# Performance work log

Measured on AMD Instinct MI355X. Metric: run time of the kernel, lower is better.

Reference implementation:

```python
import jax, jax.numpy as jnp
import numpy as np

N, D, H, F = 50000, 128, 8, 512
HD = D // H
EPS_BN = 1e-5


def _batchnorm(x, gamma, beta):
    # BatchNorm1d in training mode: per-feature batch stats over node dim
    m = x.mean(axis=0)
    v = x.var(axis=0)
    return (x - m) * jax.lax.rsqrt(v + EPS_BN) * gamma + beta


def setup_inputs() -> dict:
    key = jax.random.key(0)
    ks = jax.random.split(key, 12)
    s = 0.05
    return {
        "src": jax.random.normal(ks[0], (N, D), jnp.float32),
        "edge_index": jax.random.randint(ks[1], (2, 800000), 0, N, jnp.int64),
        "q_w": jax.random.normal(ks[2], (D, D), jnp.float32) * s,
        "q_b": jnp.zeros((D,), jnp.float32),
        "k_w": jax.random.normal(ks[3], (D, D), jnp.float32) * s,
        "v_w": jax.random.normal(ks[4], (D, D), jnp.float32) * s,
        "out_w": jax.random.normal(ks[5], (D, D), jnp.float32) * s,
        "out_b": jnp.zeros((D,), jnp.float32),
        "g1": jnp.ones((D,), jnp.float32),
        "b1": jnp.zeros((D,), jnp.float32),
        "lin1_w": jax.random.normal(ks[6], (F, D), jnp.float32) * s,
        "lin1_b": jnp.zeros((F,), jnp.float32),
        "lin2_w": jax.random.normal(ks[7], (D, F), jnp.float32) * s,
        "lin2_b": jnp.zeros((D,), jnp.float32),
        "g2": jnp.ones((D,), jnp.float32),
        "b2": jnp.zeros((D,), jnp.float32),
    }


def reference(src, edge_index, q_w, q_b, k_w, v_w, out_w, out_b,
              g1, b1, lin1_w, lin1_b, lin2_w, lin2_b, g2, b2):
    n = src.shape[0]
    # add self loops, then attention edge index is (dst=edge[1], src=edge[0])
    loops = jnp.arange(n, dtype=edge_index.dtype)
    ei = jnp.concatenate([edge_index, jnp.stack([loops, loops])], axis=1)
    e_src, e_dst = ei[0], ei[1]  # message flows e_src -> e_dst; query index = e_dst

    scaling = float(HD) ** (-0.5)
    q = ((src @ q_w.T + q_b) * scaling).reshape(n, H, HD)
    k = (src @ k_w.T).reshape(n, H, HD)
    v = (src @ v_w.T).reshape(n, H, HD)

    # per-edge scores [E, H]
    w = jnp.einsum("ehd,ehd->eh", q[e_dst], k[e_src])
    # deterministic segment softmax over edges grouped by destination node
    mx = jax.ops.segment_max(w, e_dst, num_segments=n)
    ex = jnp.exp(w - mx[e_dst])
    den = jax.ops.segment_sum(ex, e_dst, num_segments=n)
    attn_w = ex / (den[e_dst] + 1e-16)  # [E, H]

    # weighted scatter-add aggregation -> [n, H, HD]
    msgs = attn_w[:, :, None] * v[e_src]
    agg = jax.ops.segment_sum(msgs, e_dst, num_segments=n)

    attn_out = agg.reshape(n, D) @ out_w.T + out_b
    x = _batchnorm(src + attn_out, g1, b1)

    ff = jax.nn.leaky_relu(x @ lin1_w.T + lin1_b, negative_slope=0.01)
    ff = ff @ lin2_w.T + lin2_b
    x = _batchnorm(x + ff, g2, b2)
    return x
```

## Files before the change

kernel.cpp:

```cpp
#include <hip/hip_runtime.h>
#include <math.h>

#define D 128
#define H 8
#define HD 16

typedef __attribute__((ext_vector_type(8))) short bf16x8;
typedef __attribute__((ext_vector_type(4))) float f32x4;

__device__ __forceinline__ ushort f2bf(float x) {
    union { float f; unsigned u; } v; v.f = x;
    unsigned r = v.u + 0x7fffu + ((v.u >> 16) & 1u);
    return (ushort)(r >> 16);
}
__device__ __forceinline__ float bflo(unsigned u) {
    union { unsigned u; float f; } x; x.u = u << 16; return x.f;
}
__device__ __forceinline__ float bfhi(unsigned u) {
    union { unsigned u; float f; } x; x.u = u & 0xffff0000u; return x.f;
}
__device__ __forceinline__ float bf2f(short s) {
    union { unsigned u; float f; } x; x.u = ((unsigned)(ushort)s) << 16; return x.f;
}

__device__ __forceinline__ float dot16(const float* qf, uint4 a, uint4 b) {
    float w;
    w  = qf[0]  * bflo(a.x) + qf[1]  * bfhi(a.x);
    w += qf[2]  * bflo(a.y) + qf[3]  * bfhi(a.y);
    w += qf[4]  * bflo(a.z) + qf[5]  * bfhi(a.z);
    w += qf[6]  * bflo(a.w) + qf[7]  * bfhi(a.w);
    w += qf[8]  * bflo(b.x) + qf[9]  * bfhi(b.x);
    w += qf[10] * bflo(b.y) + qf[11] * bfhi(b.y);
    w += qf[12] * bflo(b.z) + qf[13] * bfhi(b.z);
    w += qf[14] * bflo(b.w) + qf[15] * bfhi(b.w);
    return w;
}
__device__ __forceinline__ void acc16(float* num, float e, uint4 a, uint4 b) {
    num[0]  = fmaf(e, bflo(a.x), num[0]);  num[1]  = fmaf(e, bfhi(a.x), num[1]);
    num[2]  = fmaf(e, bflo(a.y), num[2]);  num[3]  = fmaf(e, bfhi(a.y), num[3]);
    num[4]  = fmaf(e, bflo(a.z), num[4]);  num[5]  = fmaf(e, bfhi(a.z), num[5]);
    num[6]  = fmaf(e, bflo(a.w), num[6]);  num[7]  = fmaf(e, bfhi(a.w), num[7]);
    num[8]  = fmaf(e, bflo(b.x), num[8]);  num[9]  = fmaf(e, bfhi(b.x), num[9]);
    num[10] = fmaf(e, bflo(b.y), num[10]); num[11] = fmaf(e, bfhi(b.y), num[11]);
    num[12] = fmaf(e, bflo(b.z), num[12]); num[13] = fmaf(e, bfhi(b.z), num[13]);
    num[14] = fmaf(e, bflo(b.w), num[14]); num[15] = fmaf(e, bfhi(b.w), num[15]);
}

template<int AMODE, int EPI, int K, int MW>
__global__ __launch_bounds__(256)
void gemm_v2_kernel(const void* __restrict__ Ap,
                    const ushort* __restrict__ W,
                    const float* __restrict__ bias,
                    const void* __restrict__ extra,
                    const float* __restrict__ stats,
                    ushort* __restrict__ outb,
                    int N)
{
    constexpr int M   = MW * 4;
    constexpr int KC  = (K < 128) ? K : 128;
    constexpr int KT  = KC / 32;
    constexpr int NKC = K / KC;

    const int lane = threadIdx.x & 63, wave = threadIdx.x >> 6;
    const int lr = lane & 15, lq = lane >> 4;
    const int row0 = blockIdx.x * 32;
    const int c0w  = wave * MW;

    int ar0 = row0 + lr;      if (ar0 > N - 1) ar0 = N - 1;
    int ar1 = row0 + 16 + lr; if (ar1 > N - 1) ar1 = N - 1;

    bf16x8 afr[2][KT];

    auto loadA = [&](int kc) {
        #pragma unroll
        for (int s = 0; s < 2; ++s) {
            int ar = s ? ar1 : ar0;
            if (AMODE == 0 || AMODE == 2) {
                const ushort* ap = (const ushort*)Ap + (size_t)ar * K + kc * KC + lq * 8;
                #pragma unroll
                for (int t = 0; t < KT; ++t) {
                    bf16x8 raw = *(const bf16x8*)(ap + t * 32);
                    if (AMODE == 0) {
                        afr[s][t] = raw;
                    } else {
                        int kb = kc * KC + t * 32 + lq * 8;
                        const float4* scp = (const float4*)(stats + 256 + kb);
                        const float4* shp = (const float4*)(stats + 384 + kb);
                        float4 sA = scp[0], sB = scp[1], hA = shp[0], hB = shp[1];
                        bf16x8 o;
                        o[0] = (short)f2bf(fmaf(bf2f(raw[0]), sA.x, hA.x));
                        o[1] = (short)f2bf(fmaf(bf2f(raw[1]), sA.y, hA.y));
                        o[2] = (short)f2bf(fmaf(bf2f(raw[2]), sA.z, hA.z));
                        o[3] = (short)f2bf(fmaf(bf2f(raw[3]), sA.w, hA.w));
                        o[4] = (short)f2bf(fmaf(bf2f(raw[4]), sB.x, hB.x));
                        o[5] = (short)f2bf(fmaf(bf2f(raw[5]), sB.y, hB.y));
                        o[6] = (short)f2bf(fmaf(bf2f(raw[6]), sB.z, hB.z));
                        o[7] = (short)f2bf(fmaf(bf2f(raw[7]), sB.w, hB.w));
                        afr[s][t] = o;
                    }
                }
            } else {
                const float* ap = (const float*)Ap + (size_t)ar * K + kc * KC + lq * 8;
                #pragma unroll
                for (int t = 0; t < KT; ++t) {
                    float4 f0 = *(const float4*)(ap + t * 32);
                    float4 f1 = *(const float4*)(ap + t * 32 + 4);
                    bf16x8 o;
                    o[0] = (short)f2bf(f0.x); o[1] = (short)f2bf(f0.y);
                    o[2] = (short)f2bf(f0.z); o[3] = (short)f2bf(f0.w);
                    o[4] = (short)f2bf(f1.x); o[5] = (short)f2bf(f1.y);
                    o[6] = (short)f2bf(f1.z); o[7] = (short)f2bf(f1.w);
                    afr[s][t] = o;
                }
            }
        }
    };

    if (NKC == 1) loadA(0);

    const float*  extf = (const float*)extra;
    const ushort* extb = (const ushort*)extra;

    #pragma unroll 1
    for (int cp = 0; cp < MW / 32; ++cp) {
        const int cbase = c0w + cp * 32;
        f32x4 acc[2][2] = {};

        #pragma unroll 1
        for (int kc = 0; kc < NKC; ++kc) {
            if (NKC > 1) loadA(kc);
            const ushort* wp0 = W + (size_t)(cbase + lr) * K + kc * KC + lq * 8;
            const ushort* wp1 = wp0 + (size_t)16 * K;
            #pragma unroll
            for (int t = 0; t < KT; ++t) {
                bf16x8 b0 = *(const bf16x8*)(wp0 + t * 32);
                bf16x8 b1 = *(const bf16x8*)(wp1 + t * 32);
                acc[0][0] = __builtin_amdgcn_mfma_f32_16x16x32_bf16(afr[0][t], b0, acc[0][0], 0, 0, 0);
                acc[1][0] = __builtin_amdgcn_mfma_f32_16x16x32_bf16(afr[1][t], b0, acc[1][0], 0, 0, 0);
                acc[0][1] = __builtin_amdgcn_mfma_f32_16x16x32_bf16(afr[0][t], b1, acc[0][1], 0, 0, 0);
                acc[1][1] = __builtin_amdgcn_mfma_f32_16x16x32_bf16(afr[1][t], b1, acc[1][1], 0, 0, 0);
            }
        }

        #pragma unroll
        for (int ct = 0; ct < 2; ++ct) {
            int col = cbase + ct * 16 + lr;
            float biasv = bias[col];
            float scv = 0.f, shv = 0.f;
            if (EPI == 4) { scv = stats[256 + col]; shv = stats[384 + col]; }
            #pragma unroll
            for (int s = 0; s < 2; ++s) {
                #pragma unroll
                for (int r = 0; r < 4; ++r) {
                    int grow = row0 + s * 16 + lq * 4 + r;
                    if (grow >= N) continue;
                    size_t o = (size_t)grow * M + col;
                    float v = acc[s][ct][r] + biasv;
                    if (EPI == 2) {
                        v = v > 0.f ? v : 0.01f * v;
                    } else if (EPI == 3) {
                        v += extf[o];
                    } else if (EPI == 4) {
                        v += fmaf(bf2f((short)extb[o]), scv, shv);
                    }
                    outb[o] = f2bf(v);
                }
            }
        }
    }
}

__global__ __launch_bounds__(256)
void convert_weights_kernel(const float* __restrict__ qw, const float* __restrict__ qb,
                            const float* __restrict__ kw, const float* __restrict__ vw,
                            const float* __restrict__ ow, const float* __restrict__ w1,
                            const float* __restrict__ w2,
                            ushort* __restrict__ wqkv, ushort* __restrict__ wout,
                            ushort* __restrict__ w1b, ushort* __restrict__ w2b,
                            float* __restrict__ bqkv)
{
    int i = blockIdx.x * 256 + threadIdx.x;
    if (i < 49152) {
        int row = i >> 7;
        float v;
        if (row < 128)      v = 0.25f * qw[i];
        else if (row < 256) v = kw[i - 16384];
        else                v = vw[i - 32768];
        wqkv[i] = f2bf(v);
        return;
    }
    int j = i - 49152;
    if (j < 16384) { wout[j] = f2bf(ow[j]); return; }
    j -= 16384;
    if (j < 65536) { w1b[j] = f2bf(w1[j]); return; }
    j -= 65536;
    if (j < 65536) { w2b[j] = f2bf(w2[j]); return; }
    j -= 65536;
    if (j < 384) bqkv[j] = (j < 128) ? 0.25f * qb[j] : 0.f;
}

__global__ __launch_bounds__(256)
void deg_count_kernel(const int* __restrict__ ei, long long E0, int* __restrict__ deg)
{
    long long e = (long long)blockIdx.x * 256 + threadIdx.x;
    if (e < E0) atomicAdd(&deg[ei[E0 + e]], 1);
}

__global__ __launch_bounds__(256)
void scan_block_sum(const int* __restrict__ deg, int n, int* __restrict__ bsum)
{
    __shared__ int sh[256];
    int i = blockIdx.x * 256 + threadIdx.x;
    sh[threadIdx.x] = (i < n) ? deg[i] : 0;
    __syncthreads();
    for (int ofs = 128; ofs > 0; ofs >>= 1) {
        if (threadIdx.x < ofs) sh[threadIdx.x] += sh[threadIdx.x + ofs];
        __syncthreads();
    }
    if (threadIdx.x == 0) bsum[blockIdx.x] = sh[0];
}

__global__ void scan_offsets(const int* __restrict__ bsum, int nb, int* __restrict__ boff)
{
    __shared__ int sh[256];
    int v = (threadIdx.x < nb) ? bsum[threadIdx.x] : 0;
    sh[threadIdx.x] = v;
    __syncthreads();
    for (int ofs = 1; ofs < 256; ofs <<= 1) {
        int t = (threadIdx.x >= ofs) ? sh[threadIdx.x - ofs] : 0;
        __syncthreads();
        sh[threadIdx.x] += t;
        __syncthreads();
    }
    if (threadIdx.x < nb) boff[threadIdx.x] = sh[threadIdx.x] - v;
}

__global__ __launch_bounds__(256)
void scan_final(const int* __restrict__ deg, int n, const int* __restrict__ boff,
                int* __restrict__ rowptr)
{
    __shared__ int sh[256];
    int i = blockIdx.x * 256 + threadIdx.x;
    int v = (i < n) ? deg[i] : 0;
    sh[threadIdx.x] = v;
    __syncthreads();
    for (int ofs = 1; ofs < 256; ofs <<= 1) {
        int t = (threadIdx.x >= ofs) ? sh[threadIdx.x - ofs] : 0;
        __syncthreads();
        sh[threadIdx.x] += t;
        __syncthreads();
    }
    if (i < n) rowptr[i] = boff[blockIdx.x] + sh[threadIdx.x] - v;
    if (i == n - 1) rowptr[n] = boff[blockIdx.x] + sh[threadIdx.x];
}

__global__ __launch_bounds__(256)
void scatter_kernel(const int* __restrict__ ei, long long E0,
                    const int* __restrict__ rowptr, int* __restrict__ cnt,
                    int* __restrict__ col)
{
    long long e = (long long)blockIdx.x * 256 + threadIdx.x;
    if (e >= E0) return;
    int s = ei[e], d = ei[E0 + e];
    int pos = rowptr[d] + atomicAdd(&cnt[d], 1);
    col[pos] = s;
}

__global__ __launch_bounds__(256)
void gat_agg_kernel(const int* __restrict__ rowptr, const int* __restrict__ col,
                    const ushort* __restrict__ qkv, ushort* __restrict__ agg, int NH)
{
    int t = blockIdx.x * 256 + threadIdx.x;
    if (t >= NH) return;
    int node = t >> 3, h = t & 7;
    const uint4* Q = (const uint4*)qkv;

    const uint4* qp = Q + (size_t)node * 48 + h * 2;
    uint4 qa = qp[0], qb = qp[1];
    float qf[16];
    qf[0]=bflo(qa.x); qf[1]=bfhi(qa.x); qf[2]=bflo(qa.y); qf[3]=bfhi(qa.y);
    qf[4]=bflo(qa.z); qf[5]=bfhi(qa.z); qf[6]=bflo(qa.w); qf[7]=bfhi(qa.w);
    qf[8]=bflo(qb.x); qf[9]=bfhi(qb.x); qf[10]=bflo(qb.y); qf[11]=bfhi(qb.y);
    qf[12]=bflo(qb.z); qf[13]=bfhi(qb.z); qf[14]=bflo(qb.w); qf[15]=bfhi(qb.w);

    float num[16];
    #pragma unroll
    for (int i = 0; i < 16; i++) num[i] = 0.f;
    float den = 0.f;

    {
        uint4 ka = qp[16], kb = qp[17], va = qp[32], vb = qp[33];
        float e = __expf(dot16(qf, ka, kb));
        den += e; acc16(num, e, va, vb);
    }

    int beg = rowptr[node], end = rowptr[node + 1];
    int j = beg;
    for (; j + 4 <= end; j += 4) {
        int s0 = col[j], s1 = col[j+1], s2 = col[j+2], s3 = col[j+3];
        const uint4* b0 = Q + (size_t)s0 * 48 + h * 2;
        const uint4* b1 = Q + (size_t)s1 * 48 + h * 2;
        const uint4* b2 = Q + (size_t)s2 * 48 + h * 2;
        const uint4* b3 = Q + (size_t)s3 * 48 + h * 2;
        uint4 ka0=b0[16], kb0=b0[17], va0=b0[32], vb0=b0[33];
        uint4 ka1=b1[16], kb1=b1[17], va1=b1[32], vb1=b1[33];
        uint4 ka2=b2[16], kb2=b2[17], va2=b2[32], vb2=b2[33];
        uint4 ka3=b3[16], kb3=b3[17], va3=b3[32], vb3=b3[33];
        float e0 = __expf(dot16(qf, ka0, kb0));
        float e1 = __expf(dot16(qf, ka1, kb1));
        float e2 = __expf(dot16(qf, ka2, kb2));
        float e3 = __expf(dot16(qf, ka3, kb3));
        den += e0 + e1 + e2 + e3;
        acc16(num, e0, va0, vb0); acc16(num, e1, va1, vb1);
        acc16(num, e2, va2, vb2); acc16(num, e3, va3, vb3);
    }
    for (; j < end; ++j) {
        int s = col[j];
        const uint4* bp = Q + (size_t)s * 48 + h * 2;
        uint4 ka = bp[16], kb = bp[17], va = bp[32], vb = bp[33];
        float e = __expf(dot16(qf, ka, kb));
        den += e; acc16(num, e, va, vb);
    }

    float inv = 1.f / (den + 1e-16f);
    uint4 o0, o1;
    o0.x = (uint)f2bf(num[0]*inv)  | ((uint)f2bf(num[1]*inv)  << 16);
    o0.y = (uint)f2bf(num[2]*inv)  | ((uint)f2bf(num[3]*inv)  << 16);
    o0.z = (uint)f2bf(num[4]*inv)  | ((uint)f2bf(num[5]*inv)  << 16);
    o0.w = (uint)f2bf(num[6]*inv)  | ((uint)f2bf(num[7]*inv)  << 16);
    o1.x = (uint)f2bf(num[8]*inv)  | ((uint)f2bf(num[9]*inv)  << 16);
    o1.y = (uint)f2bf(num[10]*inv) | ((uint)f2bf(num[11]*inv) << 16);
    o1.z = (uint)f2bf(num[12]*inv) | ((uint)f2bf(num[13]*inv) << 16);
    o1.w = (uint)f2bf(num[14]*inv) | ((uint)f2bf(num[15]*inv) << 16);
    uint4* op = reinterpret_cast<uint4*>(agg + (size_t)node * 128 + h * 16);
    op[0] = o0; op[1] = o1;
}

__global__ __launch_bounds__(256)
void bn_stats_bf16_kernel(const ushort* __restrict__ y, int N, float* __restrict__ stats)
{
    int jp = threadIdx.x & 63;
    int q4 = threadIdx.x >> 6;
    int r = blockIdx.x * 256 + q4;
    int rend = min(N, (int)(blockIdx.x + 1) * 256);
    float s0 = 0.f, qq0 = 0.f, s1 = 0.f, qq1 = 0.f;
    const uint* yp = (const uint*)y;
    for (; r < rend; r += 4) {
        uint u = yp[(size_t)r * 64 + jp];
        float a = bflo(u), b = bfhi(u);
        s0 += a; qq0 += a * a; s1 += b; qq1 += b * b;
    }
    __shared__ float sh[4][64][4];
    sh[q4][jp][0] = s0; sh[q4][jp][1] = qq0; sh[q4][jp][2] = s1; sh[q4][jp][3] = qq1;
    __syncthreads();
    if (threadIdx.x < 128) {
        int p = threadIdx.x >> 1;
        int w = threadIdx.x & 1;
        float ss = 0.f, sq = 0.f;
        #pragma unroll
        for (int i = 0; i < 4; i++) { ss += sh[i][p][w * 2]; sq += sh[i][p][w * 2 + 1]; }
        unsafeAtomicAdd(&stats[2 * p + w], ss);
        unsafeAtomicAdd(&stats[128 + 2 * p + w], sq);
    }
}

__global__ void bn_finalize_kernel(float* __restrict__ stats,
                                   const float* __restrict__ g,
                                   const float* __restrict__ b, int N)
{
    int j = threadIdx.x;
    float mean = stats[j] / (float)N;
    float var  = stats[128 + j] / (float)N - mean * mean;
    float sc = g[j] * rsqrtf(var + 1e-5f);
    stats[256 + j] = sc;
    stats[384 + j] = b[j] - mean * sc;
}

__global__ __launch_bounds__(256)
void bn_apply_out_kernel(const ushort* __restrict__ y, const float* __restrict__ stats,
                         float* __restrict__ out, int total4)
{
    int i = blockIdx.x * 256 + threadIdx.x;
    if (i >= total4) return;
    uint2 u = reinterpret_cast<const uint2*>(y)[i];
    int j = (i * 4) & (D - 1);
    float4 v;
    v.x = bflo(u.x) * stats[256 + j + 0] + stats[384 + j + 0];
    v.y = bfhi(u.x) * stats[256 + j + 1] + stats[384 + j + 1];
    v.z = bflo(u.y) * stats[256 + j + 2] + stats[384 + j + 2];
    v.w = bfhi(u.y) * stats[256 + j + 3] + stats[384 + j + 3];
    reinterpret_cast<float4*>(out)[i] = v;
}

extern "C" void kernel_launch(void* const* d_in, const int* in_sizes, int n_in,
                              void* d_out, int out_size, void* d_ws, size_t ws_size,
                              hipStream_t stream)
{
    const float* src    = (const float*)d_in[0];
    const int*   ei     = (const int*)  d_in[1];
    const float* q_w    = (const float*)d_in[2];
    const float* q_b    = (const float*)d_in[3];
    const float* k_w    = (const float*)d_in[4];
    const float* v_w    = (const float*)d_in[5];
    const float* out_w  = (const float*)d_in[6];
    const float* out_b  = (const float*)d_in[7];
    const float* g1     = (const float*)d_in[8];
    const float* b1     = (const float*)d_in[9];
    const float* lin1_w = (const float*)d_in[10];
    const float* lin1_b = (const float*)d_in[11];
    const float* lin2_w = (const float*)d_in[12];
    const float* lin2_b = (const float*)d_in[13];
    const float* g2     = (const float*)d_in[14];
    const float* b2     = (const float*)d_in[15];

    const int N        = in_sizes[0] / D;
    const long long E0 = in_sizes[1] / 2;

    float* ws = (float*)d_ws;
    size_t off = 0;
    ushort* qkv  = (ushort*)(ws + off); off += (size_t)N * 192;
    ushort* agg  = (ushort*)(ws + off); off += (size_t)N * 64;
    ushort* y1b  = (ushort*)(ws + off); off += (size_t)N * 64;
    ushort* hid  = (ushort*)(ws + off); off += (size_t)N * 256;
    ushort* y2b  = (ushort*)(ws + off); off += (size_t)N * 64;
    ushort* wqkv = (ushort*)(ws + off); off += 24576;
    ushort* woutb= (ushort*)(ws + off); off += 8192;
    ushort* w1b  = (ushort*)(ws + off); off += 32768;
    ushort* w2b  = (ushort*)(ws + off); off += 32768;
    float*  bqkv = ws + off;            off += 384;
    size_t zero_start = off;
    int* deg    = (int*)(ws + off); off += N;
    int* cnt    = (int*)(ws + off); off += N;
    float* stats1 = ws + off; off += 512;
    float* stats2 = ws + off; off += 512;
    size_t zero_cnt = off - zero_start;
    int* rowptr = (int*)(ws + off); off += N + 1;
    int* bsum   = (int*)(ws + off); off += 256;
    int* boff   = (int*)(ws + off); off += 256;
    int* col    = (int*)(ws + off); off += E0;

    hipMemsetAsync(ws + zero_start, 0, zero_cnt * sizeof(float), stream);

    dim3 blk(256);

    int cw_total = 49152 + 16384 + 65536 + 65536 + 384;
    hipLaunchKernelGGL(convert_weights_kernel, dim3((cw_total + 255) / 256), blk, 0, stream,
                       q_w, q_b, k_w, v_w, out_w, lin1_w, lin2_w,
                       wqkv, woutb, w1b, w2b, bqkv);

    dim3 gE0((unsigned)((E0 + 255) / 256));
    hipLaunchKernelGGL(deg_count_kernel, gE0, blk, 0, stream, ei, E0, deg);
    int nb = (N + 255) / 256;
    hipLaunchKernelGGL(scan_block_sum, dim3(nb), blk, 0, stream, deg, N, bsum);
    hipLaunchKernelGGL(scan_offsets, dim3(1), blk, 0, stream, bsum, nb, boff);
    hipLaunchKernelGGL(scan_final, dim3(nb), blk, 0, stream, deg, N, boff, rowptr);
    hipLaunchKernelGGL(scatter_kernel, gE0, blk, 0, stream, ei, E0, rowptr, cnt, col);

    dim3 gG((N + 31) / 32);

    hipLaunchKernelGGL((gemm_v2_kernel<1, 0, 128, 96>), gG, blk, 0, stream,
                       src, wqkv, bqkv, nullptr, nullptr, qkv, N);

    int NH = N * H;
    hipLaunchKernelGGL(gat_agg_kernel, dim3((NH + 255) / 256), blk, 0, stream,
                       rowptr, col, qkv, agg, NH);

    hipLaunchKernelGGL((gemm_v2_kernel<0, 3, 128, 32>), gG, blk, 0, stream,
                       agg, woutb, out_b, src, nullptr, y1b, N);

    dim3 gS((N + 255) / 256);
    hipLaunchKernelGGL(bn_stats_bf16_kernel, gS, blk, 0, stream, y1b, N, stats1);
    hipLaunchKernelGGL(bn_finalize_kernel, dim3(1), dim3(128), 0, stream, stats1, g1, b1, N);

    hipLaunchKernelGGL((gemm_v2_kernel<2, 2, 128, 128>), gG, blk, 0, stream,
                       y1b, w1b, lin1_b, nullptr, stats1, hid, N);
    hipLaunchKernelGGL((gemm_v2_kernel<0, 4, 512, 32>), gG, blk, 0, stream,
                       hid, w2b, lin2_b, y1b, stats1, y2b, N);

    hipLaunchKernelGGL(bn_stats_bf16_kernel, gS, blk, 0, stream, y2b, N, stats2);
    hipLaunchKernelGGL(bn_finalize_kernel, dim3(1), dim3(128), 0, stream, stats2, g2, b2, N);
    int total4 = N * D / 4;
    hipLaunchKernelGGL(bn_apply_out_kernel, dim3((total4 + 255) / 256), blk, 0, stream,
                       y2b, stats2, (float*)d_out, total4);
}
```

Measured before the change: 477.2 us.

## Fuse FFN GEMMs, fold BN stats into GEMM epilogues, parallelize edge aggregation

Several changes land together. The two FFN GEMMs are merged into one kernel that keeps the hidden activations in shared memory, so the N x 512 intermediate never goes to global memory. BatchNorm statistics are now accumulated with atomics in the GEMM epilogues and finalized by the last block through a ticket counter, which removes the separate stats and finalize kernels. The QKV GEMM writes a bf16 copy of src for the residual add. The GAT aggregation splits each node's edges across 8 lanes and reduces them with shuffles, and the scan offsets kernel is folded into scan_final. Together these cut launches and HBM traffic, at the cost of more atomics, a last-block fence dependency, and a bf16 residual for src.

```diff
diff --git a/kernel.cpp b/kernel.cpp
--- a/kernel.cpp
+++ b/kernel.cpp
@@ -46,108 +46,84 @@
     num[14] = fmaf(e, bflo(b.w), num[14]); num[15] = fmaf(e, bfhi(b.w), num[15]);
 }
 
-template<int AMODE, int EPI, int K, int MW>
+template<int AMODE, int EPI, int K, int MW, bool WRITEA, bool STATF>
 __global__ __launch_bounds__(256)
 void gemm_v2_kernel(const void* __restrict__ Ap,
                     const ushort* __restrict__ W,
                     const float* __restrict__ bias,
                     const void* __restrict__ extra,
-                    const float* __restrict__ stats,
                     ushort* __restrict__ outb,
+                    ushort* __restrict__ abf,
+                    float* __restrict__ ostats, int* __restrict__ ticket,
+                    const float* __restrict__ g, const float* __restrict__ bb,
                     int N)
 {
-    constexpr int M   = MW * 4;
-    constexpr int KC  = (K < 128) ? K : 128;
-    constexpr int KT  = KC / 32;
-    constexpr int NKC = K / KC;
+    constexpr int M  = MW * 4;
+    constexpr int KT = K / 32;
 
     const int lane = threadIdx.x & 63, wave = threadIdx.x >> 6;
     const int lr = lane & 15, lq = lane >> 4;
     const int row0 = blockIdx.x * 32;
     const int c0w  = wave * MW;
 
-    int ar0 = row0 + lr;      if (ar0 > N - 1) ar0 = N - 1;
-    int ar1 = row0 + 16 + lr; if (ar1 > N - 1) ar1 = N - 1;
+    int ar0 = min(row0 + lr, N - 1);
+    int ar1 = min(row0 + 16 + lr, N - 1);
 
     bf16x8 afr[2][KT];
-
-    auto loadA = [&](int kc) {
+    #pragma unroll
+    for (int s = 0; s < 2; ++s) {
+        int ar = s ? ar1 : ar0;
+        if (AMODE == 0) {
+            const ushort* ap = (const ushort*)Ap + (size_t)ar * K + lq * 8;
+            #pragma unroll
+            for (int t = 0; t < KT; ++t) afr[s][t] = *(const bf16x8*)(ap + t * 32);
+        } else {
+            const float* ap = (const float*)Ap + (size_t)ar * K + lq * 8;
+            #pragma unroll
+            for (int t = 0; t < KT; ++t) {
+                float4 f0 = *(const float4*)(ap + t * 32);
+                float4 f1 = *(const float4*)(ap + t * 32 + 4);
+                bf16x8 o;
+                o[0] = (short)f2bf(f0.x); o[1] = (short)f2bf(f0.y);
+                o[2] = (short)f2bf(f0.z); o[3] = (short)f2bf(f0.w);
+                o[4] = (short)f2bf(f1.x); o[5] = (short)f2bf(f1.y);
+                o[6] = (short)f2bf(f1.z); o[7] = (short)f2bf(f1.w);
+                afr[s][t] = o;
+            }
+        }
+    }
+    if (WRITEA && wave == 0) {
         #pragma unroll
         for (int s = 0; s < 2; ++s) {
             int ar = s ? ar1 : ar0;
-            if (AMODE == 0 || AMODE == 2) {
-                const ushort* ap = (const ushort*)Ap + (size_t)ar * K + kc * KC + lq * 8;
-                #pragma unroll
-                for (int t = 0; t < KT; ++t) {
-                    bf16x8 raw = *(const bf16x8*)(ap + t * 32);
-                    if (AMODE == 0) {
-                        afr[s][t] = raw;
-                    } else {
-                        int kb = kc * KC + t * 32 + lq * 8;
-                        const float4* scp = (const float4*)(stats + 256 + kb);
-                        const float4* shp = (const float4*)(stats + 384 + kb);
-                        float4 sA = scp[0], sB = scp[1], hA = shp[0], hB = shp[1];
-                        bf16x8 o;
-                        o[0] = (short)f2bf(fmaf(bf2f(raw[0]), sA.x, hA.x));
-                        o[1] = (short)f2bf(fmaf(bf2f(raw[1]), sA.y, hA.y));
-                        o[2] = (short)f2bf(fmaf(bf2f(raw[2]), sA.z, hA.z));
-                        o[3] = (short)f2bf(fmaf(bf2f(raw[3]), sA.w, hA.w));
-                        o[4] = (short)f2bf(fmaf(bf2f(raw[4]), sB.x, hB.x));
-                        o[5] = (short)f2bf(fmaf(bf2f(raw[5]), sB.y, hB.y));
-                        o[6] = (short)f2bf(fmaf(bf2f(raw[6]), sB.z, hB.z));
-                        o[7] = (short)f2bf(fmaf(bf2f(raw[7]), sB.w, hB.w));
-                        afr[s][t] = o;
-                    }
-                }
-            } else {
-                const float* ap = (const float*)Ap + (size_t)ar * K + kc * KC + lq * 8;
-                #pragma unroll
-                for (int t = 0; t < KT; ++t) {
-                    float4 f0 = *(const float4*)(ap + t * 32);
-                    float4 f1 = *(const float4*)(ap + t * 32 + 4);
-                    bf16x8 o;
-                    o[0] = (short)f2bf(f0.x); o[1] = (short)f2bf(f0.y);
-                    o[2] = (short)f2bf(f0.z); o[3] = (short)f2bf(f0.w);
-                    o[4] = (short)f2bf(f1.x); o[5] = (short)f2bf(f1.y);
-                    o[6] = (short)f2bf(f1.z); o[7] = (short)f2bf(f1.w);
-                    afr[s][t] = o;
-                }
-            }
-        }
-    };
-
-    if (NKC == 1) loadA(0);
-
-    const float*  extf = (const float*)extra;
+            #pragma unroll
+            for (int t = 0; t < KT; ++t)
+                *(bf16x8*)(abf + (size_t)ar * K + t * 32 + lq * 8) = afr[s][t];
+        }
+    }
+
     const ushort* extb = (const ushort*)extra;
+    float cs[2] = {0.f, 0.f}, cq[2] = {0.f, 0.f};
 
     #pragma unroll 1
     for (int cp = 0; cp < MW / 32; ++cp) {
         const int cbase = c0w + cp * 32;
         f32x4 acc[2][2] = {};
-
-        #pragma unroll 1
-        for (int kc = 0; kc < NKC; ++kc) {
-            if (NKC > 1) loadA(kc);
-            const ushort* wp0 = W + (size_t)(cbase + lr) * K + kc * KC + lq * 8;
-            const ushort* wp1 = wp0 + (size_t)16 * K;
-            #pragma unroll
-            for (int t = 0; t < KT; ++t) {
-                bf16x8 b0 = *(const bf16x8*)(wp0 + t * 32);
-                bf16x8 b1 = *(const bf16x8*)(wp1 + t * 32);
-                acc[0][0] = __builtin_amdgcn_mfma_f32_16x16x32_bf16(afr[0][t], b0, acc[0][0], 0, 0, 0);
-                acc[1][0] = __builtin_amdgcn_mfma_f32_16x16x32_bf16(afr[1][t], b0, acc[1][0], 0, 0, 0);
-                acc[0][1] = __builtin_amdgcn_mfma_f32_16x16x32_bf16(afr[0][t], b1, acc[0][1], 0, 0, 0);
-                acc[1][1] = __builtin_amdgcn_mfma_f32_16x16x32_bf16(afr[1][t], b1, acc[1][1], 0, 0, 0);
-            }
-        }
-
+        const ushort* wp0 = W + (size_t)(cbase + lr) * K + lq * 8;
+        const ushort* wp1 = wp0 + (size_t)16 * K;
+        #pragma unroll
+        for (int t = 0; t < KT; ++t) {
+            bf16x8 b0 = *(const bf16x8*)(wp0 + t * 32);
+            bf16x8 b1 = *(const bf16x8*)(wp1 + t * 32);
+            acc[0][0] = __builtin_amdgcn_mfma_f32_16x16x32_bf16(afr[0][t], b0, acc[0][0], 0, 0, 0);
+            acc[1][0] = __builtin_amdgcn_mfma_f32_16x16x32_bf16(afr[1][t], b0, acc[1][0], 0, 0, 0);
+            acc[0][1] = __builtin_amdgcn_mfma_f32_16x16x32_bf16(afr[0][t], b1, acc[0][1], 0, 0, 0);
+            acc[1][1] = __builtin_amdgcn_mfma_f32_16x16x32_bf16(afr[1][t], b1, acc[1][1], 0, 0, 0);
+        }
         #pragma unroll
         for (int ct = 0; ct < 2; ++ct) {
             int col = cbase + ct * 16 + lr;
             float biasv = bias[col];
-            float scv = 0.f, shv = 0.f;
-            if (EPI == 4) { scv = stats[256 + col]; shv = stats[384 + col]; }
             #pragma unroll
             for (int s = 0; s < 2; ++s) {
                 #pragma unroll
@@ -156,17 +132,178 @@
                     if (grow >= N) continue;
                     size_t o = (size_t)grow * M + col;
                     float v = acc[s][ct][r] + biasv;
-                    if (EPI == 2) {
-                        v = v > 0.f ? v : 0.01f * v;
-                    } else if (EPI == 3) {
-                        v += extf[o];
-                    } else if (EPI == 4) {
-                        v += fmaf(bf2f((short)extb[o]), scv, shv);
-                    }
+                    if (EPI == 5) v += bf2f((short)extb[o]);
                     outb[o] = f2bf(v);
+                    if (STATF) { cs[ct] += v; cq[ct] += v * v; }
                 }
             }
         }
+    }
+
+    if (STATF) {
+        #pragma unroll
+        for (int ct = 0; ct < 2; ++ct) {
+            float a = cs[ct], q = cq[ct];
+            a += __shfl_xor(a, 16, 64); q += __shfl_xor(q, 16, 64);
+            a += __shfl_xor(a, 32, 64); q += __shfl_xor(q, 32, 64);
+            if (lq == 0) {
+                int col = c0w + ct * 16 + lr;
+                unsafeAtomicAdd(&ostats[col], a);
+                unsafeAtomicAdd(&ostats[128 + col], q);
+            }
+        }
+        __threadfence();
+        __syncthreads();
+        __shared__ int isl;
+        if (threadIdx.x == 0) isl = (atomicAdd(ticket, 1) == (int)gridDim.x - 1);
+        __syncthreads();
+        if (isl && threadIdx.x < 128) {
+            __threadfence();
+            int j = threadIdx.x;
+            float sm = __hip_atomic_load(&ostats[j], __ATOMIC_RELAXED, __HIP_MEMORY_SCOPE_AGENT);
+            float sq = __hip_atomic_load(&ostats[128 + j], __ATOMIC_RELAXED, __HIP_MEMORY_SCOPE_AGENT);
+            float mean = sm / (float)N;
+            float var  = sq / (float)N - mean * mean;
+            float sc = g[j] * rsqrtf(var + 1e-5f);
+            ostats[256 + j] = sc;
+            ostats[384 + j] = bb[j] - mean * sc;
+        }
+    }
+}
+
+__global__ __launch_bounds__(256)
+void ffn_fused_kernel(const ushort* __restrict__ y1b,
+                      const ushort* __restrict__ w1b, const float* __restrict__ lb1,
+                      const ushort* __restrict__ w2b, const float* __restrict__ lb2,
+                      const float* __restrict__ stats1,
+                      float* __restrict__ stats2, int* __restrict__ ticket,
+                      const float* __restrict__ g2, const float* __restrict__ b2,
+                      ushort* __restrict__ y2b, int N)
+{
+    __shared__ ushort hid[64 * 32 * 8];
+    const int lane = threadIdx.x & 63, wave = threadIdx.x >> 6;
+    const int lr = lane & 15, lq = lane >> 4;
+    const int row0 = blockIdx.x * 32;
+    int ar0 = min(row0 + lr, N - 1);
+    int ar1 = min(row0 + 16 + lr, N - 1);
+
+    bf16x8 xfr[2][4];
+    #pragma unroll
+    for (int s = 0; s < 2; ++s) {
+        int ar = s ? ar1 : ar0;
+        const ushort* ap = y1b + (size_t)ar * 128 + lq * 8;
+        #pragma unroll
+        for (int t = 0; t < 4; ++t) {
+            bf16x8 raw = *(const bf16x8*)(ap + t * 32);
+            int kb = t * 32 + lq * 8;
+            const float4* scp = (const float4*)(stats1 + 256 + kb);
+            const float4* shp = (const float4*)(stats1 + 384 + kb);
+            float4 sA = scp[0], sB = scp[1], hA = shp[0], hB = shp[1];
+            bf16x8 o;
+            o[0] = (short)f2bf(fmaf(bf2f(raw[0]), sA.x, hA.x));
+            o[1] = (short)f2bf(fmaf(bf2f(raw[1]), sA.y, hA.y));
+            o[2] = (short)f2bf(fmaf(bf2f(raw[2]), sA.z, hA.z));
+            o[3] = (short)f2bf(fmaf(bf2f(raw[3]), sA.w, hA.w));
+            o[4] = (short)f2bf(fmaf(bf2f(raw[4]), sB.x, hB.x));
+            o[5] = (short)f2bf(fmaf(bf2f(raw[5]), sB.y, hB.y));
+            o[6] = (short)f2bf(fmaf(bf2f(raw[6]), sB.z, hB.z));
+            o[7] = (short)f2bf(fmaf(bf2f(raw[7]), sB.w, hB.w));
+            xfr[s][t] = o;
+        }
+    }
+
+    #pragma unroll 1
+    for (int kb16 = 0; kb16 < 8; ++kb16) {
+        int kbase = wave * 128 + kb16 * 16;
+        const ushort* wp = w1b + (size_t)(kbase + lr) * 128 + lq * 8;
+        f32x4 a0 = {0.f,0.f,0.f,0.f}, a1 = {0.f,0.f,0.f,0.f};
+        #pragma unroll
+        for (int t = 0; t < 4; ++t) {
+            bf16x8 wf = *(const bf16x8*)(wp + t * 32);
+            a0 = __builtin_amdgcn_mfma_f32_16x16x32_bf16(wf, xfr[0][t], a0, 0, 0, 0);
+            a1 = __builtin_amdgcn_mfma_f32_16x16x32_bf16(wf, xfr[1][t], a1, 0, 0, 0);
+        }
+        float4 bi = *(const float4*)(lb1 + kbase + lq * 4);
+        int k0 = kbase + lq * 4;
+        int base0 = ((k0 >> 3) * 32) * 8 + (k0 & 7);
+        float v0, v1, v2, v3;
+        ushort4 p;
+        v0 = a0[0] + bi.x; v0 = v0 > 0.f ? v0 : 0.01f * v0;
+        v1 = a0[1] + bi.y; v1 = v1 > 0.f ? v1 : 0.01f * v1;
+        v2 = a0[2] + bi.z; v2 = v2 > 0.f ? v2 : 0.01f * v2;
+        v3 = a0[3] + bi.w; v3 = v3 > 0.f ? v3 : 0.01f * v3;
+        p.x = f2bf(v0); p.y = f2bf(v1); p.z = f2bf(v2); p.w = f2bf(v3);
+        *(ushort4*)&hid[base0 + lr * 8] = p;
+        v0 = a1[0] + bi.x; v0 = v0 > 0.f ? v0 : 0.01f * v0;
+        v1 = a1[1] + bi.y; v1 = v1 > 0.f ? v1 : 0.01f * v1;
+        v2 = a1[2] + bi.z; v2 = v2 > 0.f ? v2 : 0.01f * v2;
+        v3 = a1[3] + bi.w; v3 = v3 > 0.f ? v3 : 0.01f * v3;
+        p.x = f2bf(v0); p.y = f2bf(v1); p.z = f2bf(v2); p.w = f2bf(v3);
+        *(ushort4*)&hid[base0 + (16 + lr) * 8] = p;
+    }
+    __syncthreads();
+
+    int cb = wave * 32;
+    f32x4 acc[2][2] = {};
+    const ushort* q0 = w2b + (size_t)(cb + lr) * 512 + lq * 8;
+    const ushort* q1 = q0 + (size_t)16 * 512;
+    #pragma unroll
+    for (int t = 0; t < 16; ++t) {
+        bf16x8 h0 = *(const bf16x8*)&hid[((t * 4 + lq) * 32 + lr) * 8];
+        bf16x8 h1 = *(const bf16x8*)&hid[((t * 4 + lq) * 32 + 16 + lr) * 8];
+        bf16x8 b0 = *(const bf16x8*)(q0 + t * 32);
+        bf16x8 b1 = *(const bf16x8*)(q1 + t * 32);
+        acc[0][0] = __builtin_amdgcn_mfma_f32_16x16x32_bf16(h0, b0, acc[0][0], 0, 0, 0);
+        acc[1][0] = __builtin_amdgcn_mfma_f32_16x16x32_bf16(h1, b0, acc[1][0], 0, 0, 0);
+        acc[0][1] = __builtin_amdgcn_mfma_f32_16x16x32_bf16(h0, b1, acc[0][1], 0, 0, 0);
+        acc[1][1] = __builtin_amdgcn_mfma_f32_16x16x32_bf16(h1, b1, acc[1][1], 0, 0, 0);
+    }
+
+    float cs[2] = {0.f, 0.f}, cq[2] = {0.f, 0.f};
+    #pragma unroll
+    for (int ct = 0; ct < 2; ++ct) {
+        int col = cb + ct * 16 + lr;
+        float biasv = lb2[col];
+        float scv = stats1[256 + col], shv = stats1[384 + col];
+        #pragma unroll
+        for (int s = 0; s < 2; ++s) {
+            #pragma unroll
+            for (int r = 0; r < 4; ++r) {
+                int grow = row0 + s * 16 + lq * 4 + r;
+                if (grow >= N) continue;
+                size_t o = (size_t)grow * 128 + col;
+                float v = acc[s][ct][r] + biasv + fmaf(bf2f((short)y1b[o]), scv, shv);
+                y2b[o] = f2bf(v);
+                cs[ct] += v; cq[ct] += v * v;
+            }
+        }
+    }
+    #pragma unroll
+    for (int ct = 0; ct < 2; ++ct) {
+        float a = cs[ct], q = cq[ct];
+        a += __shfl_xor(a, 16, 64); q += __shfl_xor(q, 16, 64);
+        a += __shfl_xor(a, 32, 64); q += __shfl_xor(q, 32, 64);
+        if (lq == 0) {
+            int col = cb + ct * 16 + lr;
+            unsafeAtomicAdd(&stats2[col], a);
+            unsafeAtomicAdd(&stats2[128 + col], q);
+        }
+    }
+    __threadfence();
+    __syncthreads();
+    __shared__ int isl;
+    if (threadIdx.x == 0) isl = (atomicAdd(ticket, 1) == (int)gridDim.x - 1);
+    __syncthreads();
+    if (isl && threadIdx.x < 128) {
+        __threadfence();
+        int j = threadIdx.x;
+        float sm = __hip_atomic_load(&stats2[j], __ATOMIC_RELAXED, __HIP_MEMORY_SCOPE_AGENT);
+        float sq = __hip_atomic_load(&stats2[128 + j], __ATOMIC_RELAXED, __HIP_MEMORY_SCOPE_AGENT);
+        float mean = sm / (float)N;
+        float var  = sq / (float)N - mean * mean;
+        float sc = g2[j] * rsqrtf(var + 1e-5f);
+        stats2[256 + j] = sc;
+        stats2[384 + j] = b2[j] - mean * sc;
     }
 }
 
@@ -220,38 +357,35 @@
     if (threadIdx.x == 0) bsum[blockIdx.x] = sh[0];
 }
 
-__global__ void scan_offsets(const int* __restrict__ bsum, int nb, int* __restrict__ boff)
-{
+__global__ __launch_bounds__(256)
+void scan_final(const int* __restrict__ deg, int n, const int* __restrict__ bsum,
+                int nb, int* __restrict__ rowptr)
+{
+    __shared__ int sb[256];
     __shared__ int sh[256];
-    int v = (threadIdx.x < nb) ? bsum[threadIdx.x] : 0;
-    sh[threadIdx.x] = v;
+    int t = threadIdx.x;
+    sb[t] = (t < nb) ? bsum[t] : 0;
     __syncthreads();
     for (int ofs = 1; ofs < 256; ofs <<= 1) {
-        int t = (threadIdx.x >= ofs) ? sh[threadIdx.x - ofs] : 0;
-        __syncthreads();
-        sh[threadIdx.x] += t;
-        __syncthreads();
-    }
-    if (threadIdx.x < nb) boff[threadIdx.x] = sh[threadIdx.x] - v;
-}
-
-__global__ __launch_bounds__(256)
-void scan_final(const int* __restrict__ deg, int n, const int* __restrict__ boff,
-                int* __restrict__ rowptr)
-{
-    __shared__ int sh[256];
-    int i = blockIdx.x * 256 + threadIdx.x;
+        int v = (t >= ofs) ? sb[t - ofs] : 0;
+        __syncthreads();
+        sb[t] += v;
+        __syncthreads();
+    }
+    int boff = (blockIdx.x == 0) ? 0 : sb[blockIdx.x - 1];
+
+    int i = blockIdx.x * 256 + t;
     int v = (i < n) ? deg[i] : 0;
-    sh[threadIdx.x] = v;
+    sh[t] = v;
     __syncthreads();
     for (int ofs = 1; ofs < 256; ofs <<= 1) {
-        int t = (threadIdx.x >= ofs) ? sh[threadIdx.x - ofs] : 0;
-        __syncthreads();
-        sh[threadIdx.x] += t;
-        __syncthreads();
-    }
-    if (i < n) rowptr[i] = boff[blockIdx.x] + sh[threadIdx.x] - v;
-    if (i == n - 1) rowptr[n] = boff[blockIdx.x] + sh[threadIdx.x];
+        int u = (t >= ofs) ? sh[t - ofs] : 0;
+        __syncthreads();
+        sh[t] += u;
+        __syncthreads();
+    }
+    if (i < n) rowptr[i] = boff + sh[t] - v;
+    if (i == n - 1) rowptr[n] = boff + sh[t];
 }
 
 __global__ __launch_bounds__(256)
@@ -268,11 +402,12 @@
 
 __global__ __launch_bounds__(256)
 void gat_agg_kernel(const int* __restrict__ rowptr, const int* __restrict__ col,
-                    const ushort* __restrict__ qkv, ushort* __restrict__ agg, int NH)
-{
-    int t = blockIdx.x * 256 + threadIdx.x;
-    if (t >= NH) return;
-    int node = t >> 3, h = t & 7;
+                    const ushort* __restrict__ qkv, ushort* __restrict__ agg, int N)
+{
+    int node = blockIdx.x * 4 + (threadIdx.x >> 6);
+    if (node >= N) return;
+    int lane = threadIdx.x & 63;
+    int es = lane >> 3, h = lane & 7;
     const uint4* Q = (const uint4*)qkv;
 
     const uint4* qp = Q + (size_t)node * 48 + h * 2;
@@ -288,92 +423,38 @@
     for (int i = 0; i < 16; i++) num[i] = 0.f;
     float den = 0.f;
 
-    {
-        uint4 ka = qp[16], kb = qp[17], va = qp[32], vb = qp[33];
-        float e = __expf(dot16(qf, ka, kb));
-        den += e; acc16(num, e, va, vb);
-    }
-
-    int beg = rowptr[node], end = rowptr[node + 1];
-    int j = beg;
-    for (; j + 4 <= end; j += 4) {
-        int s0 = col[j], s1 = col[j+1], s2 = col[j+2], s3 = col[j+3];
-        const uint4* b0 = Q + (size_t)s0 * 48 + h * 2;
-        const uint4* b1 = Q + (size_t)s1 * 48 + h * 2;
-        const uint4* b2 = Q + (size_t)s2 * 48 + h * 2;
-        const uint4* b3 = Q + (size_t)s3 * 48 + h * 2;
-        uint4 ka0=b0[16], kb0=b0[17], va0=b0[32], vb0=b0[33];
-        uint4 ka1=b1[16], kb1=b1[17], va1=b1[32], vb1=b1[33];
-        uint4 ka2=b2[16], kb2=b2[17], va2=b2[32], vb2=b2[33];
-        uint4 ka3=b3[16], kb3=b3[17], va3=b3[32], vb3=b3[33];
-        float e0 = __expf(dot16(qf, ka0, kb0));
-        float e1 = __expf(dot16(qf, ka1, kb1));
-        float e2 = __expf(dot16(qf, ka2, kb2));
-        float e3 = __expf(dot16(qf, ka3, kb3));
-        den += e0 + e1 + e2 + e3;
-        acc16(num, e0, va0, vb0); acc16(num, e1, va1, vb1);
-        acc16(num, e2, va2, vb2); acc16(num, e3, va3, vb3);
-    }
-    for (; j < end; ++j) {
-        int s = col[j];
-        const uint4* bp = Q + (size_t)s * 48 + h * 2;
-        uint4 ka = bp[16], kb = bp[17], va = bp[32], vb = bp[33];
-        float e = __expf(dot16(qf, ka, kb));
-        den += e; acc16(num, e, va, vb);
-    }
-
-    float inv = 1.f / (den + 1e-16f);
-    uint4 o0, o1;
-    o0.x = (uint)f2bf(num[0]*inv)  | ((uint)f2bf(num[1]*inv)  << 16);
-    o0.y = (uint)f2bf(num[2]*inv)  | ((uint)f2bf(num[3]*inv)  << 16);
-    o0.z = (uint)f2bf(num[4]*inv)  | ((uint)f2bf(num[5]*inv)  << 16);
-    o0.w = (uint)f2bf(num[6]*inv)  | ((uint)f2bf(num[7]*inv)  << 16);
-    o1.x = (uint)f2bf(num[8]*inv)  | ((uint)f2bf(num[9]*inv)  << 16);
-    o1.y = (uint)f2bf(num[10]*inv) | ((uint)f2bf(num[11]*inv) << 16);
-    o1.z = (uint)f2bf(num[12]*inv) | ((uint)f2bf(num[13]*inv) << 16);
-    o1.w = (uint)f2bf(num[14]*inv) | ((uint)f2bf(num[15]*inv) << 16);
-    uint4* op = reinterpret_cast<uint4*>(agg + (size_t)node * 128 + h * 16);
-    op[0] = o0; op[1] = o1;
-}
-
-__global__ __launch_bounds__(256)
-void bn_stats_bf16_kernel(const ushort* __restrict__ y, int N, float* __restrict__ stats)
-{
-    int jp = threadIdx.x & 63;
-    int q4 = threadIdx.x >> 6;
-    int r = blockIdx.x * 256 + q4;
-    int rend = min(N, (int)(blockIdx.x + 1) * 256);
-    float s0 = 0.f, qq0 = 0.f, s1 = 0.f, qq1 = 0.f;
-    const uint* yp = (const uint*)y;
-    for (; r < rend; r += 4) {
-        uint u = yp[(size_t)r * 64 + jp];
-        float a = bflo(u), b = bfhi(u);
-        s0 += a; qq0 += a * a; s1 += b; qq1 += b * b;
-    }
-    __shared__ float sh[4][64][4];
-    sh[q4][jp][0] = s0; sh[q4][jp][1] = qq0; sh[q4][jp][2] = s1; sh[q4][jp][3] = qq1;
-    __syncthreads();
-    if (threadIdx.x < 128) {
-        int p = threadIdx.x >> 1;
-        int w = threadIdx.x & 1;
-        float ss = 0.f, sq = 0.f;
-        #pragma unroll
-        for (int i = 0; i < 4; i++) { ss += sh[i][p][w * 2]; sq += sh[i][p][w * 2 + 1]; }
-        unsafeAtomicAdd(&stats[2 * p + w], ss);
-        unsafeAtomicAdd(&stats[128 + 2 * p + w], sq);
-    }
-}
-
-__global__ void bn_finalize_kernel(float* __restrict__ stats,
-                                   const float* __restrict__ g,
-                                   const float* __restrict__ b, int N)
-{
-    int j = threadIdx.x;
-    float mean = stats[j] / (float)N;
-    float var  = stats[128 + j] / (float)N - mean * mean;
-    float sc = g[j] * rsqrtf(var + 1e-5f);
-    stats[256 + j] = sc;
-    stats[384 + j] = b[j] - mean * sc;
+    int beg = rowptr[node];
+    int total = rowptr[node + 1] - beg + 1;
+    for (int idx = es; idx < total; idx += 8) {
+        int s = (idx == 0) ? node : col[beg + idx - 1];
+        const uint4* rp = Q + (size_t)s * 48 + h * 2;
+        uint4 ka = rp[16], kb = rp[17], va = rp[32], vb = rp[33];
+        float ev = __expf(dot16(qf, ka, kb));
+        den += ev;
+        acc16(num, ev, va, vb);
+    }
+
+    #pragma unroll
+    for (int m = 8; m < 64; m <<= 1) {
+        den += __shfl_xor(den, m, 64);
+        #pragma unroll
+        for (int i = 0; i < 16; i++) num[i] += __shfl_xor(num[i], m, 64);
+    }
+
+    if (es == 0) {
+        float inv = 1.f / (den + 1e-16f);
+        uint4 o0, o1;
+        o0.x = (uint)f2bf(num[0]*inv)  | ((uint)f2bf(num[1]*inv)  << 16);
+        o0.y = (uint)f2bf(num[2]*inv)  | ((uint)f2bf(num[3]*inv)  << 16);
+        o0.z = (uint)f2bf(num[4]*inv)  | ((uint)f2bf(num[5]*inv)  << 16);
+        o0.w = (uint)f2bf(num[6]*inv)  | ((uint)f2bf(num[7]*inv)  << 16);
+        o1.x = (uint)f2bf(num[8]*inv)  | ((uint)f2bf(num[9]*inv)  << 16);
+        o1.y = (uint)f2bf(num[10]*inv) | ((uint)f2bf(num[11]*inv) << 16);
+        o1.z = (uint)f2bf(num[12]*inv) | ((uint)f2bf(num[13]*inv) << 16);
+        o1.w = (uint)f2bf(num[14]*inv) | ((uint)f2bf(num[15]*inv) << 16);
+        uint4* op = (uint4*)(agg + (size_t)node * 128 + h * 16);
+        op[0] = o0; op[1] = o1;
+    }
 }
 
 __global__ __launch_bounds__(256)
@@ -418,25 +499,25 @@
 
     float* ws = (float*)d_ws;
     size_t off = 0;
-    ushort* qkv  = (ushort*)(ws + off); off += (size_t)N * 192;
-    ushort* agg  = (ushort*)(ws + off); off += (size_t)N * 64;
-    ushort* y1b  = (ushort*)(ws + off); off += (size_t)N * 64;
-    ushort* hid  = (ushort*)(ws + off); off += (size_t)N * 256;
-    ushort* y2b  = (ushort*)(ws + off); off += (size_t)N * 64;
-    ushort* wqkv = (ushort*)(ws + off); off += 24576;
-    ushort* woutb= (ushort*)(ws + off); off += 8192;
-    ushort* w1b  = (ushort*)(ws + off); off += 32768;
-    ushort* w2b  = (ushort*)(ws + off); off += 32768;
-    float*  bqkv = ws + off;            off += 384;
+    ushort* qkv   = (ushort*)(ws + off); off += (size_t)N * 192;
+    ushort* agg   = (ushort*)(ws + off); off += (size_t)N * 64;
+    ushort* srcbf = (ushort*)(ws + off); off += (size_t)N * 64;
+    ushort* y1b   = (ushort*)(ws + off); off += (size_t)N * 64;
+    ushort* y2b   = (ushort*)(ws + off); off += (size_t)N * 64;
+    ushort* wqkv  = (ushort*)(ws + off); off += 24576;
+    ushort* woutb = (ushort*)(ws + off); off += 8192;
+    ushort* w1b   = (ushort*)(ws + off); off += 32768;
+    ushort* w2b   = (ushort*)(ws + off); off += 32768;
+    float*  bqkv  = ws + off;            off += 384;
     size_t zero_start = off;
     int* deg    = (int*)(ws + off); off += N;
     int* cnt    = (int*)(ws + off); off += N;
     float* stats1 = ws + off; off += 512;
     float* stats2 = ws + off; off += 512;
+    int* tickets  = (int*)(ws + off); off += 2;
     size_t zero_cnt = off - zero_start;
     int* rowptr = (int*)(ws + off); off += N + 1;
     int* bsum   = (int*)(ws + off); off += 256;
-    int* boff   = (int*)(ws + off); off += 256;
     int* col    = (int*)(ws + off); off += E0;
 
     hipMemsetAsync(ws + zero_start, 0, zero_cnt * sizeof(float), stream);
@@ -452,33 +533,26 @@
     hipLaunchKernelGGL(deg_count_kernel, gE0, blk, 0, stream, ei, E0, deg);
     int nb = (N + 255) / 256;
     hipLaunchKernelGGL(scan_block_sum, dim3(nb), blk, 0, stream, deg, N, bsum);
-    hipLaunchKernelGGL(scan_offsets, dim3(1), blk, 0, stream, bsum, nb, boff);
-    hipLaunchKernelGGL(scan_final, dim3(nb), blk, 0, stream, deg, N, boff, rowptr);
+    hipLaunchKernelGGL(scan_final, dim3(nb), blk, 0, stream, deg, N, bsum, nb, rowptr);
     hipLaunchKernelGGL(scatter_kernel, gE0, blk, 0, stream, ei, E0, rowptr, cnt, col);
 
     dim3 gG((N + 31) / 32);
 
-    hipLaunchKernelGGL((gemm_v2_kernel<1, 0, 128, 96>), gG, blk, 0, stream,
-                       src, wqkv, bqkv, nullptr, nullptr, qkv, N);
-
-    int NH = N * H;
-    hipLaunchKernelGGL(gat_agg_kernel, dim3((NH + 255) / 256), blk, 0, stream,
-                       rowptr, col, qkv, agg, NH);
-
-    hipLaunchKernelGGL((gemm_v2_kernel<0, 3, 128, 32>), gG, blk, 0, stream,
-                       agg, woutb, out_b, src, nullptr, y1b, N);
-
-    dim3 gS((N + 255) / 256);
-    hipLaunchKernelGGL(bn_stats_bf16_kernel, gS, blk, 0, stream, y1b, N, stats1);
-    hipLaunchKernelGGL(bn_finalize_kernel, dim3(1), dim3(128), 0, stream, stats1, g1, b1, N);
-
-    hipLaunchKernelGGL((gemm_v2_kernel<2, 2, 128, 128>), gG, blk, 0, stream,
-                       y1b, w1b, lin1_b, nullptr, stats1, hid, N);
-    hipLaunchKernelGGL((gemm_v2_kernel<0, 4, 512, 32>), gG, blk, 0, stream,
-                       hid, w2b, lin2_b, y1b, stats1, y2b, N);
-
-    hipLaunchKernelGGL(bn_stats_bf16_kernel, gS, blk, 0, stream, y2b, N, stats2);
-    hipLaunchKernelGGL(bn_finalize_kernel, dim3(1), dim3(128), 0, stream, stats2, g2, b2, N);
+    hipLaunchKernelGGL((gemm_v2_kernel<1, 0, 128, 96, true, false>), gG, blk, 0, stream,
+                       src, wqkv, bqkv, nullptr, qkv, srcbf,
+                       nullptr, nullptr, nullptr, nullptr, N);
+
+    hipLaunchKernelGGL(gat_agg_kernel, dim3((N + 3) / 4), blk, 0, stream,
+                       rowptr, col, qkv, agg, N);
+
+    hipLaunchKernelGGL((gemm_v2_kernel<0, 5, 128, 32, false, true>), gG, blk, 0, stream,
+                       agg, woutb, out_b, srcbf, y1b, nullptr,
+                       stats1, &tickets[0], g1, b1, N);
+
+    hipLaunchKernelGGL(ffn_fused_kernel, gG, blk, 0, stream,
+                       y1b, w1b, lin1_b, w2b, lin2_b, stats1,
+                       stats2, &tickets[1], g2, b2, y2b, N);
+
     int total4 = N * D / 4;
     hipLaunchKernelGGL(bn_apply_out_kernel, dim3((total4 + 255) / 256), blk, 0, stream,
                        y2b, stats2, (float*)d_out, total4);
```

New measurement: 673.7 us. 1.41x slower.
